# Kernel tuning notes

Hardware: AMD Instinct MI355X
Metric: run time of the kernel (lower is better)

The kernel has to match this reference:

```python
import jax, jax.numpy as jnp
import numpy as np
from jax import lax

EPS = 1e-5
N_CROPS = 501
CROP_W = 500
RF = 65          # temporal receptive field
KS = 15          # conv1 kernel size
POOL = 3


def _bn(x, g, b, m, v, axis=1):
    shp = [1] * x.ndim
    shp[axis] = -1
    inv = g.reshape(shp) / jnp.sqrt(v.reshape(shp) + EPS)
    return (x - m.reshape(shp)) * inv + b.reshape(shp)


def setup_inputs() -> dict:
    key = jax.random.key(0)
    ks = jax.random.split(key, 16)
    B, C_IN, CH, T = 16, 1, 22, 1001
    F = 36
    OUT = 4
    FLAT = F * 43  # 1548 (corrected fc in_features; repo constant 504 is inconsistent)
    d = {
        "x": jax.random.normal(ks[0], (B, C_IN, CH, T), jnp.float32),
        # temporal conv [1,65]
        "w_t": jax.random.normal(ks[1], (F, 1, 1, RF), jnp.float32) * 0.1,
        "b_t": jax.random.normal(ks[2], (F,), jnp.float32) * 0.1,
        "bn_t_g": jax.random.uniform(ks[3], (F,), jnp.float32, 0.5, 1.5),
        "bn_t_b": jax.random.normal(ks[4], (F,), jnp.float32) * 0.1,
        "bn_t_m": jax.random.normal(ks[5], (F,), jnp.float32) * 0.1,
        "bn_t_v": jax.random.uniform(ks[6], (F,), jnp.float32, 0.5, 1.5),
        # spatial conv [22,1]
        "w_s": jax.random.normal(ks[7], (F, F, CH, 1), jnp.float32) * 0.05,
        "b_s": jax.random.normal(ks[8], (F,), jnp.float32) * 0.1,
        "bn_s_g": jax.random.uniform(ks[9], (F,), jnp.float32, 0.5, 1.5),
        "bn_s_b": jax.random.normal(ks[10], (F,), jnp.float32) * 0.1,
        "bn_s_m": jax.random.normal(ks[11], (F,), jnp.float32) * 0.1,
        "bn_s_v": jax.random.uniform(ks[12], (F,), jnp.float32, 0.5, 1.5),
        # conv1 [1,15] (as 1-D conv over time)
        "w_c": jax.random.normal(ks[13], (F, F, KS), jnp.float32) * 0.05,
        "b_c": jax.random.normal(ks[14], (F,), jnp.float32) * 0.1,
        "bn_c_g": jnp.ones((F,), jnp.float32),
        "bn_c_b": jnp.zeros((F,), jnp.float32),
        "bn_c_m": jnp.zeros((F,), jnp.float32),
        "bn_c_v": jnp.ones((F,), jnp.float32),
        # fc
        "w_fc": jax.random.normal(ks[15], (OUT, FLAT), jnp.float32) * 0.02,
        "b_fc": jnp.zeros((OUT,), jnp.float32),
    }
    return d


def reference(x, w_t, b_t, bn_t_g, bn_t_b, bn_t_m, bn_t_v,
              w_s, b_s, bn_s_g, bn_s_b, bn_s_m, bn_s_v,
              w_c, b_c, bn_c_g, bn_c_b, bn_c_m, bn_c_v,
              w_fc, b_fc):
    B = x.shape[0]
    F = w_t.shape[0]
    OUT = b_fc.shape[0]

    # temporal + spatial conv/BN/ELU are shift-invariant -> compute once over full T
    h = lax.conv_general_dilated(x, w_t, (1, 1), 'VALID',
                                 dimension_numbers=('NCHW', 'OIHW', 'NCHW'))
    h = h + b_t[None, :, None, None]                       # [B,36,22,937]
    h = jax.nn.elu(_bn(h, bn_t_g, bn_t_b, bn_t_m, bn_t_v))
    h = lax.conv_general_dilated(h, w_s, (1, 1), 'VALID',
                                 dimension_numbers=('NCHW', 'OIHW', 'NCHW'))
    h = h + b_s[None, :, None, None]                       # [B,36,1,937]
    h = jax.nn.elu(_bn(h, bn_s_g, bn_s_b, bn_s_m, bn_s_v))
    h = h[:, :, 0, :]                                      # [B,36,937]

    TW = CROP_W - RF + 1  # 436: temporal width of each crop after temporal conv

    def crop_logits(i):
        sl = lax.dynamic_slice_in_dim(h, i, TW, axis=2)    # [B,36,436]
        p1 = sl[:, :, :435].reshape(B, F, 145, POOL).mean(-1)  # avgpool1 -> [B,36,145]
        c = lax.conv_general_dilated(p1, w_c, (1,), 'VALID',
                                     dimension_numbers=('NCH', 'OIH', 'NCH'))
        c = c + b_c[None, :, None]                          # [B,36,131]
        c = jax.nn.elu(_bn(c, bn_c_g, bn_c_b, bn_c_m, bn_c_v))
        p2 = c[:, :, :129].reshape(B, F, 43, POOL).mean(-1)  # avgpool2 -> [B,36,43]
        flat = p2.reshape(B, -1)                            # [B,1548]
        return flat @ w_fc.T + b_fc                         # [B,OUT]

    def step(acc, i):
        return acc + crop_logits(i), None

    init = jnp.zeros((B, OUT), x.dtype)
    total, _ = lax.scan(step, init, jnp.arange(N_CROPS))
    return total / N_CROPS
```

## Files before the change

kernel.cpp:

```cpp
#include <hip/hip_runtime.h>

#define EPS 1e-5f
#define B 16
#define CH 22
#define T_IN 1001
#define F 36
#define RF 65
#define T1 937
#define FC 792
#define KSPLIT 4
#define FCH 198
#define FSPLIT 2
#define FH 18
#define UN 885
#define UT 64
#define NU 14
#define PS_LEN 106
#define KS 15
#define GN 295
#define WN 129
#define M43 43

#define H2P_OFF 0
#define EP_OFF  2158848
#define S_OFF   3178368
#define WTT_OFF 3203136
#define WST_OFF 3205476
#define WCT_OFF 3233988
#define H1_OFF  3253440

__device__ __forceinline__ float elu_f(float v) {
    return v > 0.f ? v : (__expf(v) - 1.f);
}

__global__ __launch_bounds__(256) void k_prep(
    const float* __restrict__ w_t, const float* __restrict__ w_s,
    const float* __restrict__ w_c, float* __restrict__ wtT,
    float* __restrict__ wsT, float* __restrict__ wcT)
{
    int i = blockIdx.x * 256 + threadIdx.x;
    if (i < F * RF)     { int k = i / F,  fi = i % F; wtT[i] = w_t[fi * RF + k]; }
    if (i < FC * F)     { int fc = i / F, fo = i % F; wsT[i] = w_s[fo * FC + fc]; }
    if (i < F * KS * F) { int fk = i / F, fo = i % F; int f = fk / KS, k = fk % KS;
                          wcT[i] = w_c[(fo * F + f) * KS + k]; }
}

__global__ __launch_bounds__(256) void k_tconv(
    const float* __restrict__ x,   const float* __restrict__ wtT,
    const float* __restrict__ b_t, const float* __restrict__ g_t,
    const float* __restrict__ be_t,const float* __restrict__ m_t,
    const float* __restrict__ v_t, float* __restrict__ h1,
    int t_base, int TS, int TSeff)
{
    const int lane = threadIdx.x & 63;
    const int fi0  = __builtin_amdgcn_readfirstlane((threadIdx.x >> 6) * 9);
    const int b = blockIdx.z, ch = blockIdx.y;
    const int tloc = blockIdx.x * 64 + lane;
    const int t  = t_base + tloc;
    const int tc = t < (T1 - 1) ? t : (T1 - 1);
    const float* xr = x + (b * CH + ch) * T_IN + tc;

    float acc[9];
    #pragma unroll
    for (int j = 0; j < 9; ++j) acc[j] = 0.f;

    #pragma unroll 5
    for (int k = 0; k < RF; ++k) {
        float xv = xr[k];
        const float* wr = wtT + k * F + fi0;
        #pragma unroll
        for (int j = 0; j < 9; ++j) acc[j] += xv * wr[j];
    }

    if (t < T1 && tloc < TSeff) {
        #pragma unroll
        for (int j = 0; j < 9; ++j) {
            int fi = fi0 + j;
            float s1 = g_t[fi] * rsqrtf(v_t[fi] + EPS);
            float o1 = (b_t[fi] - m_t[fi]) * s1 + be_t[fi];
            h1[((size_t)(b * F + fi) * CH + ch) * TS + tloc] =
                elu_f(acc[j] * s1 + o1);
        }
    }
}

__global__ __launch_bounds__(256) void k_sconv(
    const float* __restrict__ h1,  const float* __restrict__ wsT,
    float* __restrict__ h2p, int t_base, int TS, int TSeff)
{
    const int lane = threadIdx.x & 63;
    const int fo0  = __builtin_amdgcn_readfirstlane((threadIdx.x >> 6) * 9);
    const int slice = blockIdx.y, b = blockIdx.z;
    const int tloc = blockIdx.x * 64 + lane;
    const int tlc  = tloc < (TSeff - 1) ? tloc : (TSeff - 1);
    const float* hr = h1 + ((size_t)b * FC + slice * FCH) * TS + tlc;
    const float* wb = wsT + slice * FCH * F;

    float acc[9];
    #pragma unroll
    for (int j = 0; j < 9; ++j) acc[j] = 0.f;

    #pragma unroll 9
    for (int fc = 0; fc < FCH; ++fc) {
        float hv = hr[(size_t)fc * TS];
        const float* wr = wb + fc * F + fo0;
        #pragma unroll
        for (int j = 0; j < 9; ++j) acc[j] += hv * wr[j];
    }

    int t = t_base + tloc;
    if (tloc < TSeff && t < T1) {
        #pragma unroll
        for (int j = 0; j < 9; ++j)
            h2p[(((size_t)slice * B + b) * F + fo0 + j) * T1 + t] = acc[j];
    }
}

__global__ __launch_bounds__(256) void k_qconv(
    const float* __restrict__ h2p, const float* __restrict__ wcT,
    const float* __restrict__ b_s, const float* __restrict__ g_s,
    const float* __restrict__ be_s,const float* __restrict__ m_s,
    const float* __restrict__ v_s, float* __restrict__ Ep)
{
    __shared__ float Ps[FH * PS_LEN];
    const int tid = threadIdx.x;
    const int slice = blockIdx.y, b = blockIdx.z;
    const int u0 = blockIdx.x * UT;
    const int f_base = slice * FH;

    for (int i = tid; i < FH * PS_LEN; i += 256) {
        int fl = i / PS_LEN, j = i % PS_LEN;
        int f = f_base + fl;
        int s = u0 + j;
        float s2 = g_s[f] * rsqrtf(v_s[f] + EPS);
        float o2 = (b_s[f] - m_s[f]) * s2 + be_s[f];
        const float* p0 = h2p + ((size_t)(0 * B + b) * F + f) * T1;
        const float* p1 = h2p + ((size_t)(1 * B + b) * F + f) * T1;
        const float* p2 = h2p + ((size_t)(2 * B + b) * F + f) * T1;
        const float* p3 = h2p + ((size_t)(3 * B + b) * F + f) * T1;
        float a = 0.f;
        #pragma unroll
        for (int d = 0; d < 3; ++d) {
            int sp = s + d;
            if (sp < T1) {
                float q = p0[sp] + p1[sp] + p2[sp] + p3[sp];
                a += elu_f(q * s2 + o2);
            }
        }
        Ps[i] = a * (1.f / 3.f);
    }
    __syncthreads();

    const int u   = tid & 63;
    const int fo0 = __builtin_amdgcn_readfirstlane((tid >> 6) * 9);

    float acc[9];
    #pragma unroll
    for (int j = 0; j < 9; ++j) acc[j] = 0.f;

    for (int fl = 0; fl < FH; ++fl) {
        const int pb = fl * PS_LEN + u;
        const int f  = f_base + fl;
        #pragma unroll
        for (int k = 0; k < KS; ++k) {
            float pv = Ps[pb + 3 * k];
            const float* wr = wcT + (f * KS + k) * F + fo0;
            #pragma unroll
            for (int j = 0; j < 9; ++j) acc[j] += pv * wr[j];
        }
    }
    int u_g = u0 + u;
    if (u_g < UN) {
        #pragma unroll
        for (int j = 0; j < 9; ++j)
            Ep[(((size_t)slice * B + b) * F + fo0 + j) * UN + u_g] = acc[j];
    }
}

__global__ __launch_bounds__(256) void k_wins(
    const float* __restrict__ Ep,  const float* __restrict__ b_c,
    const float* __restrict__ g_c, const float* __restrict__ be_c,
    const float* __restrict__ m_c, const float* __restrict__ v_c,
    float* __restrict__ S)
{
    __shared__ float Es[UN];
    __shared__ float G[GN];
    __shared__ float Ws[WN];
    const int tid = threadIdx.x;
    const int bf = blockIdx.x;
    const int f = bf % F;
    const float sc = g_c[f] * rsqrtf(v_c[f] + EPS);
    const float oc = (b_c[f] - m_c[f]) * sc + be_c[f];
    const float* e0 = Ep + (size_t)bf * UN;
    const float* e1 = Ep + ((size_t)B * F + bf) * UN;
    for (int i = tid; i < UN; i += 256)
        Es[i] = elu_f((e0[i] + e1[i]) * sc + oc);
    __syncthreads();
    for (int q = tid; q < GN; q += 256)
        G[q] = Es[3 * q] + Es[3 * q + 1] + Es[3 * q + 2];
    __syncthreads();
    if (tid < WN) {
        float a = 0.f;
        for (int q = tid; q < tid + 167; ++q) a += G[q];
        Ws[tid] = a;
    }
    __syncthreads();
    if (tid < M43)
        S[bf * M43 + tid] = (Ws[3 * tid] + Ws[3 * tid + 1] + Ws[3 * tid + 2]) * (1.f / 3.f);
}

__global__ __launch_bounds__(256) void k_fc(
    const float* __restrict__ S, const float* __restrict__ w_fc,
    const float* __restrict__ b_fc, float* __restrict__ out)
{
    const int b = blockIdx.x;
    const int o = threadIdx.x >> 6;
    const int lane = threadIdx.x & 63;
    float acc = 0.f;
    for (int n = lane; n < F * M43; n += 64)
        acc += w_fc[o * (F * M43) + n] * S[b * (F * M43) + n];
    #pragma unroll
    for (int off = 32; off > 0; off >>= 1)
        acc += __shfl_down(acc, off, 64);
    if (lane == 0) out[b * 4 + o] = acc * (1.f / 501.f) + b_fc[o];
}

extern "C" void kernel_launch(void* const* d_in, const int* in_sizes, int n_in,
                              void* d_out, int out_size, void* d_ws, size_t ws_size,
                              hipStream_t stream) {
    const float* x    = (const float*)d_in[0];
    const float* w_t  = (const float*)d_in[1];
    const float* b_t  = (const float*)d_in[2];
    const float* g_t  = (const float*)d_in[3];
    const float* be_t = (const float*)d_in[4];
    const float* m_t  = (const float*)d_in[5];
    const float* v_t  = (const float*)d_in[6];
    const float* w_s  = (const float*)d_in[7];
    const float* b_s  = (const float*)d_in[8];
    const float* g_s  = (const float*)d_in[9];
    const float* be_s = (const float*)d_in[10];
    const float* m_s  = (const float*)d_in[11];
    const float* v_s  = (const float*)d_in[12];
    const float* w_c  = (const float*)d_in[13];
    const float* b_c  = (const float*)d_in[14];
    const float* g_c  = (const float*)d_in[15];
    const float* be_c = (const float*)d_in[16];
    const float* m_c  = (const float*)d_in[17];
    const float* v_c  = (const float*)d_in[18];
    const float* w_fc = (const float*)d_in[19];
    const float* b_fc = (const float*)d_in[20];

    float* ws  = (float*)d_ws;
    float* h2p = ws + H2P_OFF;
    float* Ep  = ws + EP_OFF;
    float* S   = ws + S_OFF;
    float* wtT = ws + WTT_OFF;
    float* wsT = ws + WST_OFF;
    float* wcT = ws + WCT_OFF;
    float* h1  = ws + H1_OFF;
    float* out = (float*)d_out;

    long long availF = (long long)(ws_size / 4) - (long long)H1_OFF;
    long long tsl = availF / (B * FC);
    int TS;
    if (tsl >= T1) TS = T1;
    else { TS = (int)(tsl & ~63LL); if (TS < 64) TS = 64; }
    int nslab = (T1 + TS - 1) / TS;

    k_prep<<<dim3(112), 256, 0, stream>>>(w_t, w_s, w_c, wtT, wsT, wcT);

    for (int sl = 0; sl < nslab; ++sl) {
        int t_base = sl * TS;
        int TSeff = T1 - t_base; if (TSeff > TS) TSeff = TS;
        int ntw = (TSeff + 63) / 64;
        k_tconv<<<dim3(ntw, CH, B), 256, 0, stream>>>(
            x, wtT, b_t, g_t, be_t, m_t, v_t, h1, t_base, TS, TSeff);
        k_sconv<<<dim3(ntw, KSPLIT, B), 256, 0, stream>>>(
            h1, wsT, h2p, t_base, TS, TSeff);
    }

    k_qconv<<<dim3(NU, FSPLIT, B), 256, 0, stream>>>(
        h2p, wcT, b_s, g_s, be_s, m_s, v_s, Ep);
    k_wins<<<B * F, 256, 0, stream>>>(Ep, b_c, g_c, be_c, m_c, v_c, S);
    k_fc<<<B, 256, 0, stream>>>(S, w_fc, b_fc, out);
}
```

Baseline: 210.1 us.

## Register-block tconv/sconv/qconv over time and split pooling into separate kernel

Temporal conv now computes 8 time positions per thread, spatial conv 4, and qconv 2, so each weight load is reused across several outputs. The BN+ELU+avgpool step that qconv used to recompute per block is moved into a new k_pool kernel that writes a pooled buffer once. qconv now splits the input channels four ways instead of two, and k_wins sums four partials. The cost is more registers per thread (up to 72 accumulators in tconv) and fewer blocks in the grid, which may lower occupancy, plus one extra launch and a larger workspace.

```diff
diff --git a/kernel.cpp b/kernel.cpp
--- a/kernel.cpp
+++ b/kernel.cpp
@@ -10,24 +10,27 @@
 #define FC 792
 #define KSPLIT 4
 #define FCH 198
-#define FSPLIT 2
-#define FH 18
+#define FSPLIT 4
+#define FH2 9
 #define UN 885
-#define UT 64
-#define NU 14
-#define PS_LEN 106
+#define UT2 128
+#define NU2 7
+#define PS_LEN2 170
+#define PSTR 944
 #define KS 15
 #define GN 295
 #define WN 129
 #define M43 43
+#define BF 576
 
 #define H2P_OFF 0
-#define EP_OFF  2158848
-#define S_OFF   3178368
-#define WTT_OFF 3203136
-#define WST_OFF 3205476
-#define WCT_OFF 3233988
-#define H1_OFF  3253440
+#define P_OFF   2158848
+#define EP_OFF  2702592
+#define S_OFF   4741632
+#define WTT_OFF 4766400
+#define WST_OFF 4768740
+#define WCT_OFF 4797252
+#define H1_OFF  4816704
 
 __device__ __forceinline__ float elu_f(float v) {
     return v > 0.f ? v : (__expf(v) - 1.f);
@@ -55,31 +58,53 @@
     const int lane = threadIdx.x & 63;
     const int fi0  = __builtin_amdgcn_readfirstlane((threadIdx.x >> 6) * 9);
     const int b = blockIdx.z, ch = blockIdx.y;
-    const int tloc = blockIdx.x * 64 + lane;
-    const int t  = t_base + tloc;
-    const int tc = t < (T1 - 1) ? t : (T1 - 1);
-    const float* xr = x + (b * CH + ch) * T_IN + tc;
-
-    float acc[9];
-    #pragma unroll
-    for (int j = 0; j < 9; ++j) acc[j] = 0.f;
+    const int tl0 = blockIdx.x * 512 + lane;
+    const float* xrow = x + (b * CH + ch) * T_IN;
+
+    const float* pm[8];
+    #pragma unroll
+    for (int m = 0; m < 8; ++m) {
+        int t = t_base + tl0 + 64 * m;
+        int tc = t < (T1 - 1) ? t : (T1 - 1);
+        pm[m] = xrow + tc;
+    }
+
+    float acc[72];
+    #pragma unroll
+    for (int i = 0; i < 72; ++i) acc[i] = 0.f;
 
     #pragma unroll 5
     for (int k = 0; k < RF; ++k) {
-        float xv = xr[k];
         const float* wr = wtT + k * F + fi0;
-        #pragma unroll
-        for (int j = 0; j < 9; ++j) acc[j] += xv * wr[j];
-    }
-
-    if (t < T1 && tloc < TSeff) {
-        #pragma unroll
-        for (int j = 0; j < 9; ++j) {
-            int fi = fi0 + j;
-            float s1 = g_t[fi] * rsqrtf(v_t[fi] + EPS);
-            float o1 = (b_t[fi] - m_t[fi]) * s1 + be_t[fi];
-            h1[((size_t)(b * F + fi) * CH + ch) * TS + tloc] =
-                elu_f(acc[j] * s1 + o1);
+        float w0 = wr[0], w1 = wr[1], w2 = wr[2], w3 = wr[3], w4 = wr[4];
+        float w5 = wr[5], w6 = wr[6], w7 = wr[7], w8 = wr[8];
+        #pragma unroll
+        for (int m = 0; m < 8; ++m) {
+            float xv = pm[m][k];
+            acc[0 * 8 + m] += xv * w0;
+            acc[1 * 8 + m] += xv * w1;
+            acc[2 * 8 + m] += xv * w2;
+            acc[3 * 8 + m] += xv * w3;
+            acc[4 * 8 + m] += xv * w4;
+            acc[5 * 8 + m] += xv * w5;
+            acc[6 * 8 + m] += xv * w6;
+            acc[7 * 8 + m] += xv * w7;
+            acc[8 * 8 + m] += xv * w8;
+        }
+    }
+
+    #pragma unroll
+    for (int j = 0; j < 9; ++j) {
+        int fi = fi0 + j;
+        float s1 = g_t[fi] * rsqrtf(v_t[fi] + EPS);
+        float o1 = (b_t[fi] - m_t[fi]) * s1 + be_t[fi];
+        float* hrow = h1 + ((size_t)(b * F + fi) * CH + ch) * TS;
+        #pragma unroll
+        for (int m = 0; m < 8; ++m) {
+            int tloc = tl0 + 64 * m;
+            int t = t_base + tloc;
+            if (tloc < TSeff && t < T1)
+                hrow[tloc] = elu_f(acc[j * 8 + m] * s1 + o1);
         }
     }
 }
@@ -91,89 +116,127 @@
     const int lane = threadIdx.x & 63;
     const int fo0  = __builtin_amdgcn_readfirstlane((threadIdx.x >> 6) * 9);
     const int slice = blockIdx.y, b = blockIdx.z;
-    const int tloc = blockIdx.x * 64 + lane;
-    const int tlc  = tloc < (TSeff - 1) ? tloc : (TSeff - 1);
-    const float* hr = h1 + ((size_t)b * FC + slice * FCH) * TS + tlc;
-    const float* wb = wsT + slice * FCH * F;
-
-    float acc[9];
-    #pragma unroll
-    for (int j = 0; j < 9; ++j) acc[j] = 0.f;
-
-    #pragma unroll 9
+    const int tl0 = blockIdx.x * 256 + lane;
+
+    int off[4];
+    #pragma unroll
+    for (int m = 0; m < 4; ++m) {
+        int tloc = tl0 + 64 * m;
+        off[m] = tloc < (TSeff - 1) ? tloc : (TSeff - 1);
+    }
+
+    const float* hq = h1 + ((size_t)b * FC + slice * FCH) * TS;
+    const float* wb = wsT + slice * FCH * F + fo0;
+
+    float acc[36];
+    #pragma unroll
+    for (int i = 0; i < 36; ++i) acc[i] = 0.f;
+
+    #pragma unroll 2
     for (int fc = 0; fc < FCH; ++fc) {
-        float hv = hr[(size_t)fc * TS];
-        const float* wr = wb + fc * F + fo0;
-        #pragma unroll
-        for (int j = 0; j < 9; ++j) acc[j] += hv * wr[j];
-    }
-
-    int t = t_base + tloc;
-    if (tloc < TSeff && t < T1) {
-        #pragma unroll
-        for (int j = 0; j < 9; ++j)
-            h2p[(((size_t)slice * B + b) * F + fo0 + j) * T1 + t] = acc[j];
+        const float* wr = wb + fc * F;
+        float w0 = wr[0], w1 = wr[1], w2 = wr[2], w3 = wr[3], w4 = wr[4];
+        float w5 = wr[5], w6 = wr[6], w7 = wr[7], w8 = wr[8];
+        #pragma unroll
+        for (int m = 0; m < 4; ++m) {
+            float hv = hq[off[m]];
+            acc[0 * 4 + m] += hv * w0;
+            acc[1 * 4 + m] += hv * w1;
+            acc[2 * 4 + m] += hv * w2;
+            acc[3 * 4 + m] += hv * w3;
+            acc[4 * 4 + m] += hv * w4;
+            acc[5 * 4 + m] += hv * w5;
+            acc[6 * 4 + m] += hv * w6;
+            acc[7 * 4 + m] += hv * w7;
+            acc[8 * 4 + m] += hv * w8;
+        }
+        hq += TS;
+    }
+
+    #pragma unroll
+    for (int j = 0; j < 9; ++j) {
+        float* erow = h2p + (((size_t)slice * B + b) * F + fo0 + j) * T1;
+        #pragma unroll
+        for (int m = 0; m < 4; ++m) {
+            int tloc = tl0 + 64 * m;
+            int t = t_base + tloc;
+            if (tloc < TSeff && t < T1) erow[t] = acc[j * 4 + m];
+        }
+    }
+}
+
+__global__ __launch_bounds__(256) void k_pool(
+    const float* __restrict__ h2p, const float* __restrict__ b_s,
+    const float* __restrict__ g_s, const float* __restrict__ be_s,
+    const float* __restrict__ m_s, const float* __restrict__ v_s,
+    float* __restrict__ P)
+{
+    const int bf = blockIdx.x;
+    const int f = bf % F;
+    const float s2 = g_s[f] * rsqrtf(v_s[f] + EPS);
+    const float o2 = (b_s[f] - m_s[f]) * s2 + be_s[f];
+    const float* p0 = h2p + ((size_t)(0 * B) * F + bf) * T1;
+    const float* p1 = h2p + ((size_t)(1 * B) * F + bf) * T1;
+    const float* p2 = h2p + ((size_t)(2 * B) * F + bf) * T1;
+    const float* p3 = h2p + ((size_t)(3 * B) * F + bf) * T1;
+    for (int u = threadIdx.x; u < PSTR; u += 256) {
+        float a = 0.f;
+        #pragma unroll
+        for (int d = 0; d < 3; ++d) {
+            int s = u + d; if (s > T1 - 1) s = T1 - 1;
+            float q = p0[s] + p1[s] + p2[s] + p3[s];
+            a += elu_f(q * s2 + o2);
+        }
+        P[(size_t)bf * PSTR + u] = a * (1.f / 3.f);
     }
 }
 
 __global__ __launch_bounds__(256) void k_qconv(
-    const float* __restrict__ h2p, const float* __restrict__ wcT,
-    const float* __restrict__ b_s, const float* __restrict__ g_s,
-    const float* __restrict__ be_s,const float* __restrict__ m_s,
-    const float* __restrict__ v_s, float* __restrict__ Ep)
-{
-    __shared__ float Ps[FH * PS_LEN];
+    const float* __restrict__ P,   const float* __restrict__ wcT,
+    float* __restrict__ Ep)
+{
+    __shared__ float Ps[FH2 * PS_LEN2];
     const int tid = threadIdx.x;
     const int slice = blockIdx.y, b = blockIdx.z;
-    const int u0 = blockIdx.x * UT;
-    const int f_base = slice * FH;
-
-    for (int i = tid; i < FH * PS_LEN; i += 256) {
-        int fl = i / PS_LEN, j = i % PS_LEN;
-        int f = f_base + fl;
-        int s = u0 + j;
-        float s2 = g_s[f] * rsqrtf(v_s[f] + EPS);
-        float o2 = (b_s[f] - m_s[f]) * s2 + be_s[f];
-        const float* p0 = h2p + ((size_t)(0 * B + b) * F + f) * T1;
-        const float* p1 = h2p + ((size_t)(1 * B + b) * F + f) * T1;
-        const float* p2 = h2p + ((size_t)(2 * B + b) * F + f) * T1;
-        const float* p3 = h2p + ((size_t)(3 * B + b) * F + f) * T1;
-        float a = 0.f;
-        #pragma unroll
-        for (int d = 0; d < 3; ++d) {
-            int sp = s + d;
-            if (sp < T1) {
-                float q = p0[sp] + p1[sp] + p2[sp] + p3[sp];
-                a += elu_f(q * s2 + o2);
+    const int u0 = blockIdx.x * UT2;
+    const int f_base = slice * FH2;
+
+    for (int i = tid; i < FH2 * PS_LEN2; i += 256) {
+        int fl = i / PS_LEN2, j = i % PS_LEN2;
+        Ps[i] = P[(size_t)(b * F + f_base + fl) * PSTR + u0 + j];
+    }
+    __syncthreads();
+
+    const int lane = tid & 63;
+    const int fo0  = __builtin_amdgcn_readfirstlane((tid >> 6) * 9);
+
+    float acc[18];
+    #pragma unroll
+    for (int i = 0; i < 18; ++i) acc[i] = 0.f;
+
+    for (int fl = 0; fl < FH2; ++fl) {
+        const int pb = fl * PS_LEN2 + lane;
+        #pragma unroll
+        for (int k = 0; k < KS; ++k) {
+            float pv0 = Ps[pb + 3 * k];
+            float pv1 = Ps[pb + 64 + 3 * k];
+            const float* wr = wcT + ((f_base + fl) * KS + k) * F + fo0;
+            #pragma unroll
+            for (int j = 0; j < 9; ++j) {
+                float w = wr[j];
+                acc[j * 2 + 0] += pv0 * w;
+                acc[j * 2 + 1] += pv1 * w;
             }
         }
-        Ps[i] = a * (1.f / 3.f);
-    }
-    __syncthreads();
-
-    const int u   = tid & 63;
-    const int fo0 = __builtin_amdgcn_readfirstlane((tid >> 6) * 9);
-
-    float acc[9];
-    #pragma unroll
-    for (int j = 0; j < 9; ++j) acc[j] = 0.f;
-
-    for (int fl = 0; fl < FH; ++fl) {
-        const int pb = fl * PS_LEN + u;
-        const int f  = f_base + fl;
-        #pragma unroll
-        for (int k = 0; k < KS; ++k) {
-            float pv = Ps[pb + 3 * k];
-            const float* wr = wcT + (f * KS + k) * F + fo0;
+    }
+    #pragma unroll
+    for (int m = 0; m < 2; ++m) {
+        int u_g = u0 + lane + 64 * m;
+        if (u_g < UN) {
             #pragma unroll
-            for (int j = 0; j < 9; ++j) acc[j] += pv * wr[j];
-        }
-    }
-    int u_g = u0 + u;
-    if (u_g < UN) {
-        #pragma unroll
-        for (int j = 0; j < 9; ++j)
-            Ep[(((size_t)slice * B + b) * F + fo0 + j) * UN + u_g] = acc[j];
+            for (int j = 0; j < 9; ++j)
+                Ep[(((size_t)slice * B + b) * F + fo0 + j) * UN + u_g] = acc[j * 2 + m];
+        }
     }
 }
 
@@ -192,9 +255,11 @@
     const float sc = g_c[f] * rsqrtf(v_c[f] + EPS);
     const float oc = (b_c[f] - m_c[f]) * sc + be_c[f];
     const float* e0 = Ep + (size_t)bf * UN;
-    const float* e1 = Ep + ((size_t)B * F + bf) * UN;
+    const float* e1 = Ep + ((size_t)1 * BF + bf) * UN;
+    const float* e2 = Ep + ((size_t)2 * BF + bf) * UN;
+    const float* e3 = Ep + ((size_t)3 * BF + bf) * UN;
     for (int i = tid; i < UN; i += 256)
-        Es[i] = elu_f((e0[i] + e1[i]) * sc + oc);
+        Es[i] = elu_f((e0[i] + e1[i] + e2[i] + e3[i]) * sc + oc);
     __syncthreads();
     for (int q = tid; q < GN; q += 256)
         G[q] = Es[3 * q] + Es[3 * q + 1] + Es[3 * q + 2];
@@ -252,6 +317,7 @@
 
     float* ws  = (float*)d_ws;
     float* h2p = ws + H2P_OFF;
+    float* P   = ws + P_OFF;
     float* Ep  = ws + EP_OFF;
     float* S   = ws + S_OFF;
     float* wtT = ws + WTT_OFF;
@@ -272,15 +338,14 @@
     for (int sl = 0; sl < nslab; ++sl) {
         int t_base = sl * TS;
         int TSeff = T1 - t_base; if (TSeff > TS) TSeff = TS;
-        int ntw = (TSeff + 63) / 64;
-        k_tconv<<<dim3(ntw, CH, B), 256, 0, stream>>>(
+        k_tconv<<<dim3((TSeff + 511) / 512, CH, B), 256, 0, stream>>>(
             x, wtT, b_t, g_t, be_t, m_t, v_t, h1, t_base, TS, TSeff);
-        k_sconv<<<dim3(ntw, KSPLIT, B), 256, 0, stream>>>(
+        k_sconv<<<dim3((TSeff + 255) / 256, KSPLIT, B), 256, 0, stream>>>(
             h1, wsT, h2p, t_base, TS, TSeff);
     }
 
-    k_qconv<<<dim3(NU, FSPLIT, B), 256, 0, stream>>>(
-        h2p, wcT, b_s, g_s, be_s, m_s, v_s, Ep);
-    k_wins<<<B * F, 256, 0, stream>>>(Ep, b_c, g_c, be_c, m_c, v_c, S);
-    k_fc<<<B, 256, 0, stream>>>(S, w_fc, b_fc, out);
-}
+    k_pool<<<dim3(BF), 256, 0, stream>>>(h2p, b_s, g_s, be_s, m_s, v_s, P);
+    k_qconv<<<dim3(NU2, FSPLIT, B), 256, 0, stream>>>(P, wcT, Ep);
+    k_wins<<<dim3(BF), 256, 0, stream>>>(Ep, b_c, g_c, be_c, m_c, v_c, S);
+    k_fc<<<dim3(B), 256, 0, stream>>>(S, w_fc, b_fc, out);
+}
```

Measured after the change: 299.5 us. 42.6% more time.
